# Kernel optimization log

Hardware: AMD Instinct MI355X
Metric: run time of the kernel (lower is better)

Reference implementation:

```python
import jax, jax.numpy as jnp
import numpy as np

N, C, T, V = 32, 64, 256, 25   # batch, channels, frames, joints
REL, OUT, K = 8, 64, 5         # rel_channels = C//8, out_channels, 5 topology branches
NU = 17                        # upper-body joints (lower = V - NU = 8)


def setup_inputs() -> dict:
    key = jax.random.key(0)
    ks = jax.random.split(key, 8)
    sC = np.float32(1.0 / np.sqrt(C))
    sR = np.float32(1.0 / np.sqrt(REL))
    return {
        "x": jax.random.normal(ks[0], (N, C, T, V), jnp.float32),
        "A": jax.random.uniform(ks[1], (K, V, V), jnp.float32),
        # stacked 1x1-conv weights for the 5 branches (conv{k}_1_1, _1_2, _2, _3, _4)
        "W11": jax.random.normal(ks[2], (K, REL, C), jnp.float32) * sC,
        "b11": jnp.zeros((K, REL), jnp.float32),
        "W12": jax.random.normal(ks[3], (K, REL, C), jnp.float32) * sC,
        "b12": jnp.zeros((K, REL), jnp.float32),
        "W2": jax.random.normal(ks[4], (K, REL, C), jnp.float32) * sC,
        "b2": jnp.zeros((K, REL), jnp.float32),
        "W3": jax.random.normal(ks[5], (K, OUT, C), jnp.float32) * sC,
        "b3": jnp.zeros((K, OUT), jnp.float32),
        "W4": jax.random.normal(ks[6], (K, OUT, REL), jnp.float32) * sR,
        "b4": jnp.zeros((K, OUT), jnp.float32),
    }


def reference(x, A, W11, b11, W12, b12, W2, b2, W3, b3, W4, b4):
    # 1x1 conv followed by mean over T commutes with the (linear) conv:
    # conv(x).mean(T) == W @ x.mean(T) + b. Pool once, reuse across branches.
    mu = jnp.mean(x[:, :, :, :NU], axis=2)   # (N, C, 17)
    ml = jnp.mean(x[:, :, :, NU:], axis=2)   # (N, C, 8)

    u11 = jnp.einsum('krc,ncv->knrv', W11, mu) + b11[:, None, :, None]  # (K,N,R,17)
    u2 = jnp.einsum('krc,ncv->knrv', W2, mu) + b2[:, None, :, None]     # (K,N,R,17)
    l12 = jnp.einsum('krc,ncv->knrv', W12, ml) + b12[:, None, :, None]  # (K,N,R,8)
    l2 = jnp.einsum('krc,ncv->knrv', W2, ml) + b2[:, None, :, None]     # (K,N,R,8)

    # pairwise-difference topology blocks
    x_a = jnp.tanh(u11[..., :, None] - u2[..., None, :])   # (K,N,R,17,17)
    x_b = jnp.tanh(u11[..., :, None] - l2[..., None, :])   # (K,N,R,17,8)
    x_c = jnp.tanh(l12[..., :, None] - u2[..., None, :])   # (K,N,R,8,17)
    x_d = jnp.tanh(l12[..., :, None] - l2[..., None, :])   # (K,N,R,8,8)

    up = jnp.concatenate([x_a, x_b], axis=-1)   # (K,N,R,17,25)
    lo = jnp.concatenate([x_c, x_d], axis=-1)   # (K,N,R,8,25)

    # the original rotates the upper blocks: branch k uses upper from branch (k+1)%5
    up_rot = jnp.concatenate([up[1:], up[:1]], axis=0)
    full = jnp.concatenate([up_rot, lo], axis=-2)  # (K,N,R,25,25)

    graphs = jnp.einsum('kor,knruv->knouv', W4, full) + b4[:, None, :, None, None]  # (K,N,O,25,25)

    alpha = jnp.ones((K,), jnp.float32)  # default branch scales
    g = graphs * alpha[:, None, None, None, None] + A[:, None, None, :, :]

    x2 = jnp.einsum('koc,nctv->knotv', W3, x) + b3[:, None, :, None, None]  # (K,N,O,T,25)
    out = jnp.einsum('knouv,knotv->notu', g, x2)  # summed over the 5 branches
    return out, graphs
```

## Files before the change

### kernel.cpp

```cpp
#include <hip/hip_runtime.h>
#include <cstdint>
#include <cstddef>

#define N_  32
#define C_  64
#define T_  256
#define V_  25
#define R_  8
#define O_  64
#define K_  5
#define NU_ 17
#define U_  25
#define CV  (C_ * V_)
#define OG  4
#define NB  (OG * 32)

#define OUT_ELEMS ((size_t)N_ * O_ * T_ * V_)

typedef __attribute__((ext_vector_type(8))) short bf16x8;
typedef __attribute__((ext_vector_type(4))) float f32x4;

static __device__ __forceinline__ unsigned short f2bf(float f) {
    union { float f; unsigned u; } c; c.f = f;
    return (unsigned short)((c.u + 0x8000u) >> 16);
}
static __device__ __forceinline__ float bf2f(unsigned short h) {
    union { unsigned u; float f; } c; c.u = ((unsigned)h) << 16; return c.f;
}
static __device__ __forceinline__ unsigned pk2(float a, float b) {
    union { float f; unsigned u; } ca, cb; ca.f = a; cb.f = b;
    return ((ca.u + 0x8000u) >> 16) | ((cb.u + 0x8000u) & 0xFFFF0000u);
}
static __device__ __forceinline__ unsigned cvtpk(float a, float b) {
    unsigned r;
    asm("v_cvt_pk_bf16_f32 %0, %1, %2" : "=v"(r) : "v"(a), "v"(b));
    return r;
}

__global__ void k_xcast(const float* __restrict__ x, unsigned short* __restrict__ xT3,
                        float* __restrict__ pp) {
    __shared__ unsigned short tile[C_][408];
    int bid = blockIdx.x;
    int n = bid >> 4, tb = bid & 15;
    int tid = threadIdx.x;
    const float* xb = x + (size_t)n * C_ * T_ * V_ + tb * 400;
#pragma unroll
    for (int it = 0; it < 25; ++it) {
        int i = it * 256 + tid;
        int c = i / 100, q = i - c * 100;
        float4 v4 = *(const float4*)(xb + (size_t)c * (T_ * V_) + q * 4);
        uint2 w;
        w.x = pk2(v4.x, v4.y);
        w.y = pk2(v4.z, v4.w);
        *(uint2*)&tile[c][q * 4] = w;
    }
    __syncthreads();
    unsigned short* dstb = xT3 + ((size_t)(n * 16 + tb) * 200) * 128;
    for (int i = tid; i < 200 * 16; i += 256) {
        int sp = i >> 4, tl = i & 15;
        int v = sp >> 3, c0 = (sp & 7) * 8;
        unsigned short h[8];
#pragma unroll
        for (int j = 0; j < 8; ++j) h[j] = tile[c0 + j][tl * 25 + v];
        uint4 pk;
        pk.x = (unsigned)h[0] | ((unsigned)h[1] << 16);
        pk.y = (unsigned)h[2] | ((unsigned)h[3] << 16);
        pk.z = (unsigned)h[4] | ((unsigned)h[5] << 16);
        pk.w = (unsigned)h[6] | ((unsigned)h[7] << 16);
        *(uint4*)(dstb + (size_t)sp * 128 + tl * 8) = pk;
    }
    float* ppd = pp + ((size_t)n * 16 + tb) * CV;
    for (int e = tid; e < CV; e += 256) {
        int c = e / 25, v = e - c * 25;
        float s = 0.f;
#pragma unroll
        for (int t = 0; t < 16; ++t) s += bf2f(tile[c][t * 25 + v]);
        ppd[e] = s;
    }
}

__global__ void k_pool(const float* __restrict__ x, float* __restrict__ pool) {
    int nc = blockIdx.x;
    int t  = threadIdx.x;
    const float* px = x + ((size_t)nc * T_ + t) * V_;
    float acc[V_];
#pragma unroll
    for (int v = 0; v < V_; ++v) acc[v] = px[v];
#pragma unroll
    for (int off = 32; off > 0; off >>= 1) {
#pragma unroll
        for (int v = 0; v < V_; ++v) acc[v] += __shfl_down(acc[v], off, 64);
    }
    __shared__ float sm[4][V_];
    int wave = t >> 6, lane = t & 63;
    if (lane == 0) {
#pragma unroll
        for (int v = 0; v < V_; ++v) sm[wave][v] = acc[v];
    }
    __syncthreads();
    if (t < V_) {
        float s = sm[0][t] + sm[1][t] + sm[2][t] + sm[3][t];
        pool[(size_t)nc * V_ + t] = s * (1.0f / T_);
    }
}

__global__ void k_tvals(const float* __restrict__ pool,
                        const float* __restrict__ W11, const float* __restrict__ b11,
                        const float* __restrict__ W12, const float* __restrict__ b12,
                        const float* __restrict__ W2,  const float* __restrict__ b2,
                        float* __restrict__ t2o, float* __restrict__ tSo) {
    int kn = blockIdx.x;
    int k = kn / N_, n = kn % N_;
    int tid = threadIdx.x;
    int r = tid >> 5, v = tid & 31;
    if (v >= V_) return;
    const float* pp = pool + (size_t)n * C_ * V_ + v;
    const float* w2 = W2 + ((size_t)k * R_ + r) * C_;
    const float* w1 = ((v < NU_) ? W11 : W12) + ((size_t)k * R_ + r) * C_;
    float a2 = b2[k * R_ + r];
    float a1 = (v < NU_) ? b11[k * R_ + r] : b12[k * R_ + r];
    for (int c = 0; c < C_; ++c) {
        float p = pp[(size_t)c * V_];
        a2 += w2[c] * p;
        a1 += w1[c] * p;
    }
    size_t idx = (((size_t)k * N_ + n) * R_ + r) * V_ + v;
    t2o[idx] = a2;
    tSo[idx] = a1;
}

__global__ void k_graphs(const float* __restrict__ t2v, const float* __restrict__ tSv,
                         const float* __restrict__ W4, const float* __restrict__ b4,
                         float* __restrict__ graphs) {
    int kn = blockIdx.x;
    int k = kn / N_, n = kn % N_;
    int kup = (k + 1) % K_;
    __shared__ float F[R_][V_ * V_];
    __shared__ float w4s[O_][R_];
    __shared__ float b4s[O_];
    int tid = threadIdx.x;
    for (int i = tid; i < O_ * R_; i += 256) w4s[i / R_][i % R_] = W4[(size_t)k * O_ * R_ + i];
    if (tid < O_) b4s[tid] = b4[k * O_ + tid];
    for (int idx = tid; idx < R_ * V_ * V_; idx += 256) {
        int r = idx / (V_ * V_), uv = idx % (V_ * V_);
        int u = uv / V_, v = uv % V_;
        int ks = (u < NU_) ? kup : k;
        size_t base = (((size_t)ks * N_ + n) * R_ + r) * V_;
        F[r][uv] = tanhf(tSv[base + u] - t2v[base + v]);
    }
    __syncthreads();
    float* gout = graphs + ((size_t)k * N_ + n) * O_ * (V_ * V_);
    for (int idx = tid; idx < O_ * V_ * V_; idx += 256) {
        int o = idx / (V_ * V_), uv = idx % (V_ * V_);
        float a = b4s[o];
#pragma unroll
        for (int r = 0; r < R_; ++r) a += w4s[o][r] * F[r][uv];
        gout[idx] = a;
    }
}

__global__ void k_graphs2c(const float* __restrict__ pp,
                           const float* __restrict__ W11, const float* __restrict__ b11,
                           const float* __restrict__ W12, const float* __restrict__ b12,
                           const float* __restrict__ W2,  const float* __restrict__ b2,
                           const float* __restrict__ W4,  const float* __restrict__ b4,
                           float* __restrict__ graphs) {
    int bid = blockIdx.x;
    int og = bid & 1;
    int kn = bid >> 1;
    int k = kn / N_, n = kn % N_;
    int kup = (k + 1) % K_;
    __shared__ float poolL[CV];
    __shared__ float t2s[2][R_][V_];
    __shared__ float tSs[2][R_][V_];
    __shared__ float F[R_][V_ * V_];
    __shared__ float w4s[O_][R_];
    __shared__ float b4s[O_];
    int tid = threadIdx.x;
    for (int i = tid; i < O_ * R_; i += 512) w4s[i / R_][i % R_] = W4[(size_t)k * O_ * R_ + i];
    if (tid < O_) b4s[tid] = b4[k * O_ + tid];
    const float* ppn = pp + (size_t)n * 16 * CV;
    for (int i = tid; i < CV; i += 512) {
        float s = 0.f;
#pragma unroll
        for (int tb = 0; tb < 16; ++tb) s += ppn[(size_t)tb * CV + i];
        poolL[i] = s * (1.0f / T_);
    }
    __syncthreads();
    for (int i = tid; i < 2 * R_ * V_; i += 512) {
        int ks = i / (R_ * V_);
        int rem = i - ks * (R_ * V_);
        int r = rem / V_, v = rem - r * V_;
        int kk = ks ? kup : k;
        const float* w2 = W2 + ((size_t)kk * R_ + r) * C_;
        const float* w1 = ((v < NU_) ? W11 : W12) + ((size_t)kk * R_ + r) * C_;
        float a2 = b2[kk * R_ + r];
        float a1 = (v < NU_) ? b11[kk * R_ + r] : b12[kk * R_ + r];
        for (int c = 0; c < C_; ++c) {
            float p = poolL[c * 25 + v];
            a2 += w2[c] * p;
            a1 += w1[c] * p;
        }
        t2s[ks][r][v] = a2;
        tSs[ks][r][v] = a1;
    }
    __syncthreads();
    for (int idx = tid; idx < R_ * V_ * V_; idx += 512) {
        int r = idx / (V_ * V_), uv = idx % (V_ * V_);
        int u = uv / V_, v = uv % V_;
        int ks = (u < NU_) ? 1 : 0;
        F[r][uv] = tanhf(tSs[ks][r][u] - t2s[ks][r][v]);
    }
    __syncthreads();
    float* gout = graphs + ((size_t)k * N_ + n) * O_ * (V_ * V_);
    const int half = O_ * V_ * V_ / 2;
    for (int idx = og * half + tid; idx < (og + 1) * half; idx += 512) {
        int o = idx / (V_ * V_), uv = idx % (V_ * V_);
        float a = b4s[o];
#pragma unroll
        for (int r = 0; r < R_; ++r) a += w4s[o][r] * F[r][uv];
        gout[idx] = a;
    }
}

__global__ __launch_bounds__(512, 4) void k_main_fast(
    const unsigned short* __restrict__ xT3,
    const float* __restrict__ graphs,
    const float* __restrict__ Adj,
    const float* __restrict__ W3,
    const float* __restrict__ b3,
    float* __restrict__ out) {

    __shared__ unsigned short Hs[2][4][NB][8];
    __shared__ f32x4 Gls4[OG * 625];
    __shared__ float Gls1[OG * 625];
    __shared__ f32x4 W3km[K_ * OG * 16];
    __shared__ float biasS[NB];

    const int tid = threadIdx.x;
    const int bid = blockIdx.x;
    const int obase = (bid & 15) * OG;
    const int n = bid >> 4;
    const int lane = tid & 63;
    const int wv_ = tid >> 6;

    const size_t kstride = (size_t)N_ * O_ * 625;
    for (int i = tid; i < OG * 625; i += 512) {
        int o = i / 625, uv = i - o * 625;
        int u = uv / 25, v = uv - u * 25;
        size_t gb = ((size_t)n * O_ + obase + o) * 625 + uv;
        f32x4 g4;
        g4[0] = graphs[gb]               + Adj[uv];
        g4[1] = graphs[gb + kstride]     + Adj[625 + uv];
        g4[2] = graphs[gb + 2 * kstride] + Adj[1250 + uv];
        g4[3] = graphs[gb + 3 * kstride] + Adj[1875 + uv];
        int idx = o * 625 + v * 25 + u;
        Gls4[idx] = g4;
        Gls1[idx] = graphs[gb + 4 * kstride] + Adj[2500 + uv];
    }
    for (int i = tid; i < K_ * OG * C_; i += 512) {
        int k = i / (OG * C_);
        int rem = i - k * (OG * C_);
        int o = rem >> 6, c = rem & 63;
        ((float*)W3km)[((k * OG + o) * C_) + c] = W3[((size_t)k * O_ + obase + o) * C_ + c];
    }
    __syncthreads();

    if (tid < NB) {
        int o = tid >> 5, u = tid & 31;
        float bv = 0.f;
        if (u < U_) {
            f32x4 s4 = {0.f, 0.f, 0.f, 0.f};
            float s5 = 0.f;
            for (int v = 0; v < V_; ++v) {
                int idx = o * 625 + v * 25 + u;
                s4 += Gls4[idx];
                s5 += Gls1[idx];
            }
            bv = s4[0] * b3[0 * O_ + obase + o] + s4[1] * b3[1 * O_ + obase + o]
               + s4[2] * b3[2 * O_ + obase + o] + s4[3] * b3[3 * O_ + obase + o]
               + s5 * b3[4 * O_ + obase + o];
        }
        biasS[tid] = bv;
    }

    const int sl = wv_ & 3;
    const int hncol = (wv_ >> 2) * 64 + lane;
    const int ho = hncol >> 5;
    const int hu = hncol & 31;
    const int kw = OG * 16;
    const f32x4* wb  = &W3km[ho * 16 + sl * 2];
    const f32x4* gp4 = &Gls4[ho * 625 + hu];
    const float* gp1 = &Gls1[ho * 625 + hu];
    uint4* hw = (uint4*)&Hs[0][sl][hncol][0];

    auto h_form = [&](uint4* hwp, const f32x4* wbp, f32x4 g, float g5) {
        f32x4 w0a = wbp[0],        w0b = wbp[1];
        f32x4 w1a = wbp[kw],       w1b = wbp[kw + 1];
        f32x4 w2a = wbp[2 * kw],   w2b = wbp[2 * kw + 1];
        f32x4 w3a = wbp[3 * kw],   w3b = wbp[3 * kw + 1];
        f32x4 w4a = wbp[4 * kw],   w4b = wbp[4 * kw + 1];
        float h[8];
#pragma unroll
        for (int j = 0; j < 4; ++j) {
            h[j]     = w0a[j] * g[0] + w1a[j] * g[1] + w2a[j] * g[2] + w3a[j] * g[3] + w4a[j] * g5;
            h[4 + j] = w0b[j] * g[0] + w1b[j] * g[1] + w2b[j] * g[2] + w3b[j] * g[3] + w4b[j] * g5;
        }
        uint4 hv;
        hv.x = cvtpk(h[0], h[1]); hv.y = cvtpk(h[2], h[3]);
        hv.z = cvtpk(h[4], h[5]); hv.w = cvtpk(h[6], h[7]);
        *hwp = hv;
    };
    auto ld_g = [&](int voff25, f32x4& g, float& g5) {
        if (hu < U_) { g = gp4[voff25]; g5 = gp1[voff25]; }
        else { g = (f32x4){0.f, 0.f, 0.f, 0.f}; g5 = 0.f; }
    };

    const int wm = wv_ >> 1;
    const int wn = wv_ & 1;
    const int lr = lane & 15;
    const int eg = lane >> 4;

    f32x4 acc[4][4];
#pragma unroll
    for (int mt = 0; mt < 4; ++mt)
#pragma unroll
        for (int nt = 0; nt < 4; ++nt) acc[mt][nt] = (f32x4){0.f, 0.f, 0.f, 0.f};

    const unsigned short* An = xT3 + (size_t)n * (T_ * CV);
    const unsigned short* a0 = An + ((size_t)((wm * 4 + 0) * 200 + eg)) * 128 + lr * 8;
    const unsigned short* a1 = a0 + 200 * 128;
    const unsigned short* a2 = a0 + 400 * 128;
    const unsigned short* a3 = a0 + 600 * 128;
    const char* hrb = (const char*)&Hs[0][eg][wn * 64 + lr][0];

    auto consume = [&](int sub , int bufb ) {
        uint4 av0 = *(const uint4*)(a0 + sub);
        uint4 av1 = *(const uint4*)(a1 + sub);
        uint4 av2 = *(const uint4*)(a2 + sub);
        uint4 av3 = *(const uint4*)(a3 + sub);
        bf16x8 b[4];
#pragma unroll
        for (int nt = 0; nt < 4; ++nt)
            b[nt] = *(const bf16x8*)(hrb + bufb + nt * 256);
        __builtin_amdgcn_s_setprio(1);
        union { uint4 u; bf16x8 h; } c0, c1, c2, c3;
        c0.u = av0; c1.u = av1; c2.u = av2; c3.u = av3;
#pragma unroll
        for (int nt = 0; nt < 4; ++nt) acc[0][nt] = __builtin_amdgcn_mfma_f32_16x16x32_bf16(c0.h, b[nt], acc[0][nt], 0, 0, 0);
#pragma unroll
        for (int nt = 0; nt < 4; ++nt) acc[1][nt] = __builtin_amdgcn_mfma_f32_16x16x32_bf16(c1.h, b[nt], acc[1][nt], 0, 0, 0);
#pragma unroll
        for (int nt = 0; nt < 4; ++nt) acc[2][nt] = __builtin_amdgcn_mfma_f32_16x16x32_bf16(c2.h, b[nt], acc[2][nt], 0, 0, 0);
#pragma unroll
        for (int nt = 0; nt < 4; ++nt) acc[3][nt] = __builtin_amdgcn_mfma_f32_16x16x32_bf16(c3.h, b[nt], acc[3][nt], 0, 0, 0);
        __builtin_amdgcn_s_setprio(0);
    };

    f32x4 gv; float gv5;
    ld_g(0, gv, gv5);
    h_form(hw, wb, gv, gv5);
    __syncthreads();

    for (int kc2 = 0; kc2 < 25; ++kc2) {
        consume(0, 0);
        h_form(hw + 512, wb + 8, gv, gv5);
        __syncthreads();
        consume(512, 8192);
        if (kc2 + 1 < 25) {
            ld_g((kc2 + 1) * 25, gv, gv5);
            h_form(hw, wb, gv, gv5);
        }
        __syncthreads();
        a0 += 1024; a1 += 1024; a2 += 1024; a3 += 1024;
    }

#pragma unroll
    for (int nt = 0; nt < 4; ++nt) {
        int ncol = wn * 64 + nt * 16 + lr;
        int ol = ncol >> 5;
        int u  = ncol & 31;
        if (u < U_) {
            float bv = biasS[ncol];
            float* ob = out + ((size_t)n * O_ + obase + ol) * T_ * V_ + u;
#pragma unroll
            for (int mt = 0; mt < 4; ++mt) {
                int t0 = wm * 64 + mt * 16 + eg * 4;
#pragma unroll
                for (int r2 = 0; r2 < 4; ++r2)
                    ob[(size_t)(t0 + r2) * V_] = acc[mt][nt][r2] + bv;
            }
        }
    }
}

#define OB 4
#define TB 64
__global__ __launch_bounds__(256, 1) void k_main_slow(
    const float* __restrict__ x, const float* __restrict__ graphs,
    const float* __restrict__ A, const float* __restrict__ W3,
    const float* __restrict__ b3, float* __restrict__ out) {
    int bid = blockIdx.x;
    int tb = bid & 3;
    int ob = (bid >> 2) & 15;
    int n  = bid >> 6;
    int tid = threadIdx.x;
    int ol = tid >> 6;
    int tl = tid & 63;
    int t = tb * TB + tl;
    int o = ob * OB + ol;

    __shared__ float Gs[K_][OB][V_][28];
    __shared__ float W3s[K_][OB][C_];
    __shared__ float b3s[K_][OB];

    for (int i = tid; i < K_ * OB * V_ * V_; i += 256) {
        int k   = i / (OB * V_ * V_);
        int rem = i % (OB * V_ * V_);
        int oo  = rem / (V_ * V_);
        int uv  = rem % (V_ * V_);
        Gs[k][oo][uv / V_][uv % V_] =
            graphs[(((size_t)k * N_ + n) * O_ + ob * OB + oo) * (V_ * V_) + uv]
            + A[k * V_ * V_ + uv];
    }
    for (int i = tid; i < K_ * OB * C_; i += 256) {
        int k   = i / (OB * C_);
        int rem = i % (OB * C_);
        int oo  = rem / C_, c = rem % C_;
        W3s[k][oo][c] = W3[((size_t)k * O_ + ob * OB + oo) * C_ + c];
    }
    if (tid < K_ * OB) b3s[tid / OB][tid % OB] = b3[(tid / OB) * O_ + ob * OB + tid % OB];
    __syncthreads();

    float x2[K_][V_];
#pragma unroll
    for (int k = 0; k < K_; ++k)
#pragma unroll
        for (int v = 0; v < V_; ++v) x2[k][v] = b3s[k][ol];

    const float* xb = x + ((size_t)n * C_ * T_ + t) * V_;
    for (int c = 0; c < C_; ++c) {
        const float* p = xb + (size_t)c * T_ * V_;
        float xv[V_];
#pragma unroll
        for (int v = 0; v < V_; ++v) xv[v] = p[v];
#pragma unroll
        for (int k = 0; k < K_; ++k) {
            float w = W3s[k][ol][c];
#pragma unroll
            for (int v = 0; v < V_; ++v) x2[k][v] += w * xv[v];
        }
    }

    float acc[V_];
#pragma unroll
    for (int u = 0; u < V_; ++u) acc[u] = 0.0f;
#pragma unroll
    for (int k = 0; k < K_; ++k) {
#pragma unroll
        for (int u = 0; u < V_; ++u) {
            const float* gr = &Gs[k][ol][u][0];
            float s = 0.0f;
#pragma unroll
            for (int v = 0; v < V_; ++v) s += gr[v] * x2[k][v];
            acc[u] += s;
        }
    }
    float* po = out + (((size_t)n * O_ + o) * T_ + t) * V_;
#pragma unroll
    for (int u = 0; u < V_; ++u) po[u] = acc[u];
}

extern "C" void kernel_launch(void* const* d_in, const int* in_sizes, int n_in,
                              void* d_out, int out_size, void* d_ws, size_t ws_size,
                              hipStream_t stream) {
    const float* x   = (const float*)d_in[0];
    const float* A   = (const float*)d_in[1];
    const float* W11 = (const float*)d_in[2];
    const float* b11 = (const float*)d_in[3];
    const float* W12 = (const float*)d_in[4];
    const float* b12 = (const float*)d_in[5];
    const float* W2  = (const float*)d_in[6];
    const float* b2  = (const float*)d_in[7];
    const float* W3  = (const float*)d_in[8];
    const float* b3  = (const float*)d_in[9];
    const float* W4  = (const float*)d_in[10];
    const float* b4  = (const float*)d_in[11];

    float* out    = (float*)d_out;
    float* graphs = out + OUT_ELEMS;

    const size_t xT_bytes = sizeof(unsigned short) * (size_t)N_ * T_ * CV;
    const size_t pp_bytes = sizeof(float) * (size_t)N_ * 16 * CV;
    const size_t hdr      = (size_t)(1 << 20);
    const bool fast = (ws_size >= hdr + xT_bytes + pp_bytes);

    const size_t poolElems = (size_t)N_ * C_ * V_;
    const size_t tElems    = (size_t)K_ * N_ * R_ * V_;
    const size_t slowNeed  = (poolElems + 2 * tElems) * sizeof(float);

    float* scratch = (fast || ws_size >= slowNeed) ? (float*)d_ws : out;
    float* pool = scratch;
    float* t2v  = scratch + poolElems;
    float* tSv  = t2v + tElems;
    unsigned short* xT3 = (unsigned short*)((char*)d_ws + hdr);
    float* pp = (float*)((char*)d_ws + hdr + xT_bytes);

    if (fast) {
        k_xcast   <<<N_ * 16, 256, 0, stream>>>(x, xT3, pp);
        k_graphs2c<<<K_ * N_ * 2, 512, 0, stream>>>(pp, W11, b11, W12, b12, W2, b2, W4, b4, graphs);
        k_main_fast<<<N_ * 16, 512, 0, stream>>>(xT3, graphs, A, W3, b3, out);
    } else {
        k_pool  <<<N_ * C_, 256, 0, stream>>>(x, pool);
        k_tvals <<<K_ * N_, 256, 0, stream>>>(pool, W11, b11, W12, b12, W2, b2, t2v, tSv);
        k_graphs<<<K_ * N_, 256, 0, stream>>>(t2v, tSv, W4, b4, graphs);
        k_main_slow<<<N_ * (O_ / OB) * 4, 256, 0, stream>>>(x, graphs, A, W3, b3, out);
    }
}
```

Before: 110.9 us.

## Split main loop into two channel-half passes with register-resident W3 weights

The reduction over channel halves is restructured into two sequential passes. Each pass loads its W3 weight vectors into registers once instead of re-reading them from LDS on every H formation. Each pass walks all 25 v steps with a double-buffered H tile and one barrier per step, where the old loop interleaved both halves with two barriers per iteration. Launch bounds drop from 4 to 2 blocks per CU to allow the extra registers, which risks lower occupancy, and the G values are reloaded from LDS twice.

Result: slower. 136.4 us (+23.0%).

```diff
diff --git a/kernel.cpp b/kernel.cpp
--- a/kernel.cpp
+++ b/kernel.cpp
@@ -223,7 +223,7 @@
     }
 }
 
-__global__ __launch_bounds__(512, 4) void k_main_fast(
+__global__ __launch_bounds__(512, 2) void k_main_fast(
     const unsigned short* __restrict__ xT3,
     const float* __restrict__ graphs,
     const float* __restrict__ Adj,
@@ -288,91 +288,98 @@
     const int hncol = (wv_ >> 2) * 64 + lane;
     const int ho = hncol >> 5;
     const int hu = hncol & 31;
-    const int kw = OG * 16;
-    const f32x4* wb  = &W3km[ho * 16 + sl * 2];
     const f32x4* gp4 = &Gls4[ho * 625 + hu];
     const float* gp1 = &Gls1[ho * 625 + hu];
     uint4* hw = (uint4*)&Hs[0][sl][hncol][0];
 
-    auto h_form = [&](uint4* hwp, const f32x4* wbp, f32x4 g, float g5) {
+    auto ld_g = [&](int voff25, f32x4& g, float& g5) {
+        if (hu < U_) { g = gp4[voff25]; g5 = gp1[voff25]; }
+        else { g = (f32x4){0.f, 0.f, 0.f, 0.f}; g5 = 0.f; }
+    };
+
+    const int wm = wv_ >> 1;
+    const int wn = wv_ & 1;
+    const int lr = lane & 15;
+    const int eg = lane >> 4;
+
+    f32x4 acc[4][4];
+#pragma unroll
+    for (int mt = 0; mt < 4; ++mt)
+#pragma unroll
+        for (int nt = 0; nt < 4; ++nt) acc[mt][nt] = (f32x4){0.f, 0.f, 0.f, 0.f};
+
+    const unsigned short* An = xT3 + (size_t)n * (T_ * CV);
+    const char* hrb = (const char*)&Hs[0][eg][wn * 64 + lr][0];
+
+    auto consume = [&](const unsigned short* pa0, const unsigned short* pa1,
+                       const unsigned short* pa2, const unsigned short* pa3,
+                       int bufb) {
+        uint4 av0 = *(const uint4*)pa0;
+        uint4 av1 = *(const uint4*)pa1;
+        uint4 av2 = *(const uint4*)pa2;
+        uint4 av3 = *(const uint4*)pa3;
+        bf16x8 b[4];
+#pragma unroll
+        for (int nt = 0; nt < 4; ++nt)
+            b[nt] = *(const bf16x8*)(hrb + bufb + nt * 256);
+        __builtin_amdgcn_s_setprio(1);
+        union { uint4 u; bf16x8 h; } c0, c1, c2, c3;
+        c0.u = av0; c1.u = av1; c2.u = av2; c3.u = av3;
+#pragma unroll
+        for (int nt = 0; nt < 4; ++nt) acc[0][nt] = __builtin_amdgcn_mfma_f32_16x16x32_bf16(c0.h, b[nt], acc[0][nt], 0, 0, 0);
+#pragma unroll
+        for (int nt = 0; nt < 4; ++nt) acc[1][nt] = __builtin_amdgcn_mfma_f32_16x16x32_bf16(c1.h, b[nt], acc[1][nt], 0, 0, 0);
+#pragma unroll
+        for (int nt = 0; nt < 4; ++nt) acc[2][nt] = __builtin_amdgcn_mfma_f32_16x16x32_bf16(c2.h, b[nt], acc[2][nt], 0, 0, 0);
+#pragma unroll
+        for (int nt = 0; nt < 4; ++nt) acc[3][nt] = __builtin_amdgcn_mfma_f32_16x16x32_bf16(c3.h, b[nt], acc[3][nt], 0, 0, 0);
+        __builtin_amdgcn_s_setprio(0);
+    };
+
+#pragma unroll
+    for (int par = 0; par < 2; ++par) {
+        const int kw = OG * 16;
+        const f32x4* wbp = &W3km[ho * 16 + par * 8 + sl * 2];
         f32x4 w0a = wbp[0],        w0b = wbp[1];
         f32x4 w1a = wbp[kw],       w1b = wbp[kw + 1];
         f32x4 w2a = wbp[2 * kw],   w2b = wbp[2 * kw + 1];
         f32x4 w3a = wbp[3 * kw],   w3b = wbp[3 * kw + 1];
         f32x4 w4a = wbp[4 * kw],   w4b = wbp[4 * kw + 1];
-        float h[8];
-#pragma unroll
-        for (int j = 0; j < 4; ++j) {
-            h[j]     = w0a[j] * g[0] + w1a[j] * g[1] + w2a[j] * g[2] + w3a[j] * g[3] + w4a[j] * g5;
-            h[4 + j] = w0b[j] * g[0] + w1b[j] * g[1] + w2b[j] * g[2] + w3b[j] * g[3] + w4b[j] * g5;
+
+        auto hform = [&](uint4* hwp, f32x4 g, float g5) {
+            float h[8];
+#pragma unroll
+            for (int j = 0; j < 4; ++j) {
+                h[j]     = w0a[j] * g[0] + w1a[j] * g[1] + w2a[j] * g[2] + w3a[j] * g[3] + w4a[j] * g5;
+                h[4 + j] = w0b[j] * g[0] + w1b[j] * g[1] + w2b[j] * g[2] + w3b[j] * g[3] + w4b[j] * g5;
+            }
+            uint4 hv;
+            hv.x = cvtpk(h[0], h[1]); hv.y = cvtpk(h[2], h[3]);
+            hv.z = cvtpk(h[4], h[5]); hv.w = cvtpk(h[6], h[7]);
+            *hwp = hv;
+        };
+
+        const unsigned short* pa0 = An + ((size_t)((wm * 4 + 0) * 200 + par * 4 + eg)) * 128 + lr * 8;
+        const unsigned short* pa1 = pa0 + 200 * 128;
+        const unsigned short* pa2 = pa0 + 400 * 128;
+        const unsigned short* pa3 = pa0 + 600 * 128;
+
+        f32x4 gv; float gv5;
+        ld_g(0, gv, gv5);
+        hform(hw, gv, gv5);
+        __syncthreads();
+
+        int hrOff = 0;
+        for (int v = 0; v < 25; ++v) {
+            consume(pa0, pa1, pa2, pa3, hrOff);
+            if (v < 24) {
+                ld_g((v + 1) * 25, gv, gv5);
+                hform((uint4*)((char*)hw + (hrOff ^ 8192)), gv, gv5);
+            }
+            __syncthreads();
+            pa0 += 1024; pa1 += 1024; pa2 += 1024; pa3 += 1024;
+            hrOff ^= 8192;
         }
-        uint4 hv;
-        hv.x = cvtpk(h[0], h[1]); hv.y = cvtpk(h[2], h[3]);
-        hv.z = cvtpk(h[4], h[5]); hv.w = cvtpk(h[6], h[7]);
-        *hwp = hv;
-    };
-    auto ld_g = [&](int voff25, f32x4& g, float& g5) {
-        if (hu < U_) { g = gp4[voff25]; g5 = gp1[voff25]; }
-        else { g = (f32x4){0.f, 0.f, 0.f, 0.f}; g5 = 0.f; }
-    };
-
-    const int wm = wv_ >> 1;
-    const int wn = wv_ & 1;
-    const int lr = lane & 15;
-    const int eg = lane >> 4;
-
-    f32x4 acc[4][4];
-#pragma unroll
-    for (int mt = 0; mt < 4; ++mt)
-#pragma unroll
-        for (int nt = 0; nt < 4; ++nt) acc[mt][nt] = (f32x4){0.f, 0.f, 0.f, 0.f};
-
-    const unsigned short* An = xT3 + (size_t)n * (T_ * CV);
-    const unsigned short* a0 = An + ((size_t)((wm * 4 + 0) * 200 + eg)) * 128 + lr * 8;
-    const unsigned short* a1 = a0 + 200 * 128;
-    const unsigned short* a2 = a0 + 400 * 128;
-    const unsigned short* a3 = a0 + 600 * 128;
-    const char* hrb = (const char*)&Hs[0][eg][wn * 64 + lr][0];
-
-    auto consume = [&](int sub , int bufb ) {
-        uint4 av0 = *(const uint4*)(a0 + sub);
-        uint4 av1 = *(const uint4*)(a1 + sub);
-        uint4 av2 = *(const uint4*)(a2 + sub);
-        uint4 av3 = *(const uint4*)(a3 + sub);
-        bf16x8 b[4];
-#pragma unroll
-        for (int nt = 0; nt < 4; ++nt)
-            b[nt] = *(const bf16x8*)(hrb + bufb + nt * 256);
-        __builtin_amdgcn_s_setprio(1);
-        union { uint4 u; bf16x8 h; } c0, c1, c2, c3;
-        c0.u = av0; c1.u = av1; c2.u = av2; c3.u = av3;
-#pragma unroll
-        for (int nt = 0; nt < 4; ++nt) acc[0][nt] = __builtin_amdgcn_mfma_f32_16x16x32_bf16(c0.h, b[nt], acc[0][nt], 0, 0, 0);
-#pragma unroll
-        for (int nt = 0; nt < 4; ++nt) acc[1][nt] = __builtin_amdgcn_mfma_f32_16x16x32_bf16(c1.h, b[nt], acc[1][nt], 0, 0, 0);
-#pragma unroll
-        for (int nt = 0; nt < 4; ++nt) acc[2][nt] = __builtin_amdgcn_mfma_f32_16x16x32_bf16(c2.h, b[nt], acc[2][nt], 0, 0, 0);
-#pragma unroll
-        for (int nt = 0; nt < 4; ++nt) acc[3][nt] = __builtin_amdgcn_mfma_f32_16x16x32_bf16(c3.h, b[nt], acc[3][nt], 0, 0, 0);
-        __builtin_amdgcn_s_setprio(0);
-    };
-
-    f32x4 gv; float gv5;
-    ld_g(0, gv, gv5);
-    h_form(hw, wb, gv, gv5);
-    __syncthreads();
-
-    for (int kc2 = 0; kc2 < 25; ++kc2) {
-        consume(0, 0);
-        h_form(hw + 512, wb + 8, gv, gv5);
-        __syncthreads();
-        consume(512, 8192);
-        if (kc2 + 1 < 25) {
-            ld_g((kc2 + 1) * 25, gv, gv5);
-            h_form(hw, wb, gv, gv5);
-        }
-        __syncthreads();
-        a0 += 1024; a1 += 1024; a2 += 1024; a3 += 1024;
     }
 
 #pragma unroll
```
